# Performance work log

Measured on AMD Instinct MI355X. Metric: run time of the kernel, lower is better.

The kernel has to match this reference:

```python
import jax, jax.numpy as jnp
import numpy as np

N, P, D = 262144, 128, 64
EPS = 1e-5
NEG = -1e30


def setup_inputs() -> dict:
    key = jax.random.key(0)
    ks = jax.random.split(key, 12)
    feature = jax.random.normal(ks[0], (N, D), jnp.float32)
    feature_geo = jax.random.normal(ks[1], (N, D), jnp.float32)
    xyz = jax.random.uniform(ks[2], (N, 3), jnp.float32)
    centers = jax.random.uniform(ks[3], (3,), jnp.float32)
    plane_center = jax.random.uniform(ks[4], (P, 3), jnp.float32)
    nrm = jax.random.normal(ks[5], (P, 3), jnp.float32)
    plane_normal = nrm / jnp.linalg.norm(nrm, axis=1, keepdims=True)
    lo = 0.3 * jax.random.uniform(ks[6], (P, 3), jnp.float32)
    hi = 0.5 + 0.5 * jax.random.uniform(ks[7], (P, 3), jnp.float32)
    # exactly two active axes per plane (one axis of the aabb is zeroed)
    ax = jnp.arange(P) % 3
    keep = (jnp.arange(3)[None, :] != ax[:, None]).astype(jnp.float32)
    plane_xyz_min = lo * keep
    plane_xyz_max = hi * keep
    w1 = 0.05 * jax.random.normal(ks[8], (2 * D, D), jnp.float32)
    b1 = jnp.zeros((D,), jnp.float32)
    w2 = 0.05 * jax.random.normal(ks[9], (D, D), jnp.float32)
    b2 = jnp.zeros((D,), jnp.float32)
    w3 = 0.05 * jax.random.normal(ks[10], (D, 1), jnp.float32)
    b3 = jnp.zeros((1,), jnp.float32)
    g1 = jnp.ones((D,), jnp.float32); be1 = jnp.zeros((D,), jnp.float32)
    m1 = jnp.zeros((D,), jnp.float32); v1 = jnp.ones((D,), jnp.float32)
    g2 = jnp.ones((D,), jnp.float32); be2 = jnp.zeros((D,), jnp.float32)
    m2 = jnp.zeros((D,), jnp.float32); v2 = jnp.ones((D,), jnp.float32)
    return dict(feature=feature, feature_geo=feature_geo, xyz=xyz, centers=centers,
                plane_center=plane_center, plane_normal=plane_normal,
                plane_xyz_min=plane_xyz_min, plane_xyz_max=plane_xyz_max,
                w1=w1, b1=b1, g1=g1, be1=be1, m1=m1, v1=v1,
                w2=w2, b2=b2, g2=g2, be2=be2, m2=m2, v2=v2,
                w3=w3, b3=b3)


def _bn(x, g, b, m, v):
    return (x - m) * (g * jax.lax.rsqrt(v + EPS)) + b


def reference(feature, feature_geo, xyz, centers, plane_center, plane_normal,
              plane_xyz_min, plane_xyz_max, w1, b1, g1, be1, m1, v1,
              w2, b2, g2, be2, m2, v2, w3, b3):
    clouds = xyz + centers                                   # [N,3]
    f = jnp.concatenate([feature, feature_geo], axis=1)      # [N,2D]
    # 1x1 conv MLP == per-point matmul (fc1 -> fc2 with BN+ReLU, fc3)
    h1 = jax.nn.relu(_bn(f @ w1 + b1, g1, be1, m1, v1))      # [N,D]
    h2 = jax.nn.relu(_bn(h1 @ w2 + b2, g2, be2, m2, v2))     # [N,D]
    scores = jax.nn.relu(h2 @ w3 + b3)[:, 0]                 # [N]
    # per-plane aabb mask over the two active axes (xyz_max != 0)
    active = plane_xyz_max != 0                              # [P,3]
    in_rng = (clouds[None] >= plane_xyz_min[:, None]) & (clouds[None] < plane_xyz_max[:, None])
    range_mask = jnp.all(in_rng | ~active[:, None, :], axis=-1)   # [P,N]
    # point-to-plane distance: |(clouds - center) . normal|
    dots = clouds @ plane_normal.T                           # [N,P]
    offs = jnp.sum(plane_center * plane_normal, axis=1)      # [P]
    dist = jnp.abs(dots - offs[None, :]).T                   # [P,N]
    mask = range_mask & (dist < 0.1)                         # [P,N]
    sig = jax.nn.sigmoid(scores)                             # [N]
    on_mask = mask & (sig > 0.5)[None, :]
    off_mask = mask & (sig <= 0.5)[None, :]

    def pool(m):  # masked max-pool of fc2 features over points of one plane
        val = jnp.max(jnp.where(m[:, None], h2, NEG), axis=0)     # [D]
        return jnp.where(jnp.any(m), val, 0.0)

    on_feat = jax.lax.map(pool, on_mask)                     # [P,D]
    off_feat = jax.lax.map(pool, off_mask)                   # [P,D]
    scores_masked = jnp.where(mask, scores[None, :], 0.0)    # [P,N]
    return scores_masked, mask, on_mask, off_mask, on_feat, off_feat
```

## Files before the change

kernel.cpp:

```cpp
#include <hip/hip_runtime.h>
#include <hip/hip_bf16.h>
#include <math.h>

#define NPTS 262144
#define NP   128
#define DD   64
#define NWORDS (NPTS / 64)

#define AS4 __attribute__((address_space(4)))
typedef float evf4 __attribute__((ext_vector_type(4)));
typedef AS4 const float* csf;
typedef AS4 const evf4*  csf4;
#define TO_CSF(p)  ((csf)(unsigned long long)(const void*)(p))
#define TO_CSF4(p) ((csf4)(unsigned long long)(const void*)(p))

__global__ __launch_bounds__(256) void prep_kernel(
    const float* __restrict__ plane_center, const float* __restrict__ plane_normal,
    const float* __restrict__ pmin, const float* __restrict__ pmax,
    const float* __restrict__ w2,
    float* __restrict__ packed, float* __restrict__ w2T,
    float* __restrict__ out_feats)
{
    const int t = threadIdx.x;
    out_feats[blockIdx.x * 256 + t] = 0.0f;
    if (blockIdx.x == 0 && t < NP) {
        float n0 = plane_normal[t*3+0], n1 = plane_normal[t*3+1], n2 = plane_normal[t*3+2];
        float c0 = plane_center[t*3+0], c1 = plane_center[t*3+1], c2 = plane_center[t*3+2];
        float off = (c0*n0 + c1*n1) + c2*n2;
        float4* pp = reinterpret_cast<float4*>(packed) + t * 3;
        pp[0] = make_float4(n0, n1, n2, off);
        pp[1] = make_float4(pmin[t*3+0], pmin[t*3+1], pmin[t*3+2], 0.0f);
        pp[2] = make_float4(pmax[t*3+0], pmax[t*3+1], pmax[t*3+2], 0.0f);
    }
    if (blockIdx.x == 1) {
#pragma unroll
        for (int u = 0; u < 16; ++u) {
            const int e = u * 256 + t;
            const int j = e >> 6, k = e & 63;
            w2T[e] = w2[k * DD + j];
        }
    }
}

__global__ __launch_bounds__(256) void fused_kernel(
    const float* __restrict__ feature, const float* __restrict__ feature_geo,
    const float* __restrict__ xyz, const float* __restrict__ centers,
    const float* __restrict__ packed,
    const float* __restrict__ w1, const float* __restrict__ b1,
    const float* __restrict__ g1, const float* __restrict__ be1,
    const float* __restrict__ m1, const float* __restrict__ v1,
    const float* __restrict__ w2T, const float* __restrict__ b2,
    const float* __restrict__ g2, const float* __restrict__ be2,
    const float* __restrict__ m2, const float* __restrict__ v2,
    const float* __restrict__ w3, const float* __restrict__ b3,
    float* __restrict__ h2_out,
    float* __restrict__ out_sm, float* __restrict__ out_mask,
    float* __restrict__ out_on, float* __restrict__ out_off,
    unsigned long long* __restrict__ hitOn, unsigned long long* __restrict__ hitOff)
{
    __shared__ float sw1[128 * DD];
    __shared__ float sw2[DD * DD];
    const int t = threadIdx.x;
    const int bs = (blockIdx.x & 7) * 128 + (blockIdx.x >> 3);
    const int n = bs * 256 + t;
    const int lane = t & 63;
    const int word = n >> 6;

    {
        const float4* s1 = reinterpret_cast<const float4*>(w1);
        const float4* s2 = reinterpret_cast<const float4*>(w2T);
        float4* d1 = reinterpret_cast<float4*>(sw1);
        float4* d2 = reinterpret_cast<float4*>(sw2);
#pragma unroll
        for (int k = 0; k < 8; ++k) d1[t + k * 256] = s1[t + k * 256];
#pragma unroll
        for (int k = 0; k < 4; ++k) d2[t + k * 256] = s2[t + k * 256];
    }

    const csf cc = TO_CSF(centers);
    const float c0 = xyz[n*3+0] + cc[0];
    const float c1 = xyz[n*3+1] + cc[1];
    const float c2 = xyz[n*3+2] + cc[2];

    __syncthreads();

    float acc[DD];
#pragma unroll
    for (int j = 0; j < DD; ++j) acc[j] = 0.0f;

    const float4* fA = reinterpret_cast<const float4*>(feature) + (size_t)n * 16;
    const float4* fB = reinterpret_cast<const float4*>(feature_geo) + (size_t)n * 16;
#pragma unroll 1
    for (int q = 0; q < 16; ++q) {
        const float4 fv = fA[q];
        const evf4* wr = reinterpret_cast<const evf4*>(sw1 + q * 4 * DD);
#pragma unroll
        for (int j4 = 0; j4 < 16; ++j4) { const evf4 w = wr[j4];
            acc[4*j4+0] = fmaf(fv.x, w.x, acc[4*j4+0]);
            acc[4*j4+1] = fmaf(fv.x, w.y, acc[4*j4+1]);
            acc[4*j4+2] = fmaf(fv.x, w.z, acc[4*j4+2]);
            acc[4*j4+3] = fmaf(fv.x, w.w, acc[4*j4+3]); }
#pragma unroll
        for (int j4 = 0; j4 < 16; ++j4) { const evf4 w = wr[16 + j4];
            acc[4*j4+0] = fmaf(fv.y, w.x, acc[4*j4+0]);
            acc[4*j4+1] = fmaf(fv.y, w.y, acc[4*j4+1]);
            acc[4*j4+2] = fmaf(fv.y, w.z, acc[4*j4+2]);
            acc[4*j4+3] = fmaf(fv.y, w.w, acc[4*j4+3]); }
#pragma unroll
        for (int j4 = 0; j4 < 16; ++j4) { const evf4 w = wr[32 + j4];
            acc[4*j4+0] = fmaf(fv.z, w.x, acc[4*j4+0]);
            acc[4*j4+1] = fmaf(fv.z, w.y, acc[4*j4+1]);
            acc[4*j4+2] = fmaf(fv.z, w.z, acc[4*j4+2]);
            acc[4*j4+3] = fmaf(fv.z, w.w, acc[4*j4+3]); }
#pragma unroll
        for (int j4 = 0; j4 < 16; ++j4) { const evf4 w = wr[48 + j4];
            acc[4*j4+0] = fmaf(fv.w, w.x, acc[4*j4+0]);
            acc[4*j4+1] = fmaf(fv.w, w.y, acc[4*j4+1]);
            acc[4*j4+2] = fmaf(fv.w, w.z, acc[4*j4+2]);
            acc[4*j4+3] = fmaf(fv.w, w.w, acc[4*j4+3]); }
    }
#pragma unroll 1
    for (int q = 0; q < 16; ++q) {
        const float4 fv = fB[q];
        const evf4* wr = reinterpret_cast<const evf4*>(sw1 + (DD + q * 4) * DD);
#pragma unroll
        for (int j4 = 0; j4 < 16; ++j4) { const evf4 w = wr[j4];
            acc[4*j4+0] = fmaf(fv.x, w.x, acc[4*j4+0]);
            acc[4*j4+1] = fmaf(fv.x, w.y, acc[4*j4+1]);
            acc[4*j4+2] = fmaf(fv.x, w.z, acc[4*j4+2]);
            acc[4*j4+3] = fmaf(fv.x, w.w, acc[4*j4+3]); }
#pragma unroll
        for (int j4 = 0; j4 < 16; ++j4) { const evf4 w = wr[16 + j4];
            acc[4*j4+0] = fmaf(fv.y, w.x, acc[4*j4+0]);
            acc[4*j4+1] = fmaf(fv.y, w.y, acc[4*j4+1]);
            acc[4*j4+2] = fmaf(fv.y, w.z, acc[4*j4+2]);
            acc[4*j4+3] = fmaf(fv.y, w.w, acc[4*j4+3]); }
#pragma unroll
        for (int j4 = 0; j4 < 16; ++j4) { const evf4 w = wr[32 + j4];
            acc[4*j4+0] = fmaf(fv.z, w.x, acc[4*j4+0]);
            acc[4*j4+1] = fmaf(fv.z, w.y, acc[4*j4+1]);
            acc[4*j4+2] = fmaf(fv.z, w.z, acc[4*j4+2]);
            acc[4*j4+3] = fmaf(fv.z, w.w, acc[4*j4+3]); }
#pragma unroll
        for (int j4 = 0; j4 < 16; ++j4) { const evf4 w = wr[48 + j4];
            acc[4*j4+0] = fmaf(fv.w, w.x, acc[4*j4+0]);
            acc[4*j4+1] = fmaf(fv.w, w.y, acc[4*j4+1]);
            acc[4*j4+2] = fmaf(fv.w, w.z, acc[4*j4+2]);
            acc[4*j4+3] = fmaf(fv.w, w.w, acc[4*j4+3]); }
    }
    {
        const csf g1c = TO_CSF(g1), v1c = TO_CSF(v1), b1c = TO_CSF(b1),
                  m1c = TO_CSF(m1), be1c = TO_CSF(be1);
#pragma unroll
        for (int j = 0; j < DD; ++j) {
            float sc = g1c[j] * (1.0f / sqrtf(v1c[j] + 1e-5f));
            float h  = fmaf(acc[j] + b1c[j] - m1c[j], sc, be1c[j]);
            acc[j] = fmaxf(h, 0.0f);
        }
    }

    const csf g2c = TO_CSF(g2), v2c = TO_CSF(v2), b2c = TO_CSF(b2),
              m2c = TO_CSF(m2), be2c = TO_CSF(be2), w3c = TO_CSF(w3);
    float s = 0.0f;
    float4* o = reinterpret_cast<float4*>(h2_out) + (size_t)n * 16;
#pragma unroll 1
    for (int jq = 0; jq < 16; ++jq) {
        const evf4* r0 = reinterpret_cast<const evf4*>(sw2 + (4*jq + 0) * DD);
        const evf4* r1 = reinterpret_cast<const evf4*>(sw2 + (4*jq + 1) * DD);
        const evf4* r2 = reinterpret_cast<const evf4*>(sw2 + (4*jq + 2) * DD);
        const evf4* r3 = reinterpret_cast<const evf4*>(sw2 + (4*jq + 3) * DD);
        float a0 = 0.0f, a1 = 0.0f, a2 = 0.0f, a3 = 0.0f;
#pragma unroll
        for (int k4 = 0; k4 < 16; ++k4) {
            const evf4 w0 = r0[k4], w1v = r1[k4], w2v = r2[k4], w3v = r3[k4];
            const float h0 = acc[4*k4+0], h1v = acc[4*k4+1],
                        h2v = acc[4*k4+2], h3v = acc[4*k4+3];
            a0 = fmaf(h0, w0.x, a0); a0 = fmaf(h1v, w0.y, a0);
            a0 = fmaf(h2v, w0.z, a0); a0 = fmaf(h3v, w0.w, a0);
            a1 = fmaf(h0, w1v.x, a1); a1 = fmaf(h1v, w1v.y, a1);
            a1 = fmaf(h2v, w1v.z, a1); a1 = fmaf(h3v, w1v.w, a1);
            a2 = fmaf(h0, w2v.x, a2); a2 = fmaf(h1v, w2v.y, a2);
            a2 = fmaf(h2v, w2v.z, a2); a2 = fmaf(h3v, w2v.w, a2);
            a3 = fmaf(h0, w3v.x, a3); a3 = fmaf(h1v, w3v.y, a3);
            a3 = fmaf(h2v, w3v.z, a3); a3 = fmaf(h3v, w3v.w, a3);
        }
        float hv[4] = {a0, a1, a2, a3};
#pragma unroll
        for (int u = 0; u < 4; ++u) {
            const int jj = 4*jq + u;
            float sc = g2c[jj] * (1.0f / sqrtf(v2c[jj] + 1e-5f));
            float h  = fmaf(hv[u] + b2c[jj] - m2c[jj], sc, be2c[jj]);
            h = fmaxf(h, 0.0f);
            hv[u] = h;
            s = fmaf(h, w3c[jj], s);
        }
        o[jq] = make_float4(hv[0], hv[1], hv[2], hv[3]);
    }
    s += TO_CSF(b3)[0];
    const float score = fmaxf(s, 0.0f);

    const bool on = (0.5f + 0.5f * tanhf(0.5f * score)) > 0.5f;

    const csf4 pp = TO_CSF4(packed);
#pragma unroll 1
    for (int p = 0; p < NP; ++p) {
        const evf4 nrm = pp[p*3+0];
        const evf4 mn  = pp[p*3+1];
        const evf4 mx  = pp[p*3+2];
        float d = fabsf(fmaf(c2, nrm.z, fmaf(c1, nrm.y, c0 * nrm.x)) - nrm.w);
        bool ok0 = (mx.x == 0.0f) | ((c0 >= mn.x) & (c0 < mx.x));
        bool ok1 = (mx.y == 0.0f) | ((c1 >= mn.y) & (c1 < mx.y));
        bool ok2 = (mx.z == 0.0f) | ((c2 >= mn.z) & (c2 < mx.z));
        bool mk  = ok0 & ok1 & ok2 & (d < 0.1f);
        const size_t idx = (size_t)p * NPTS + n;
        const bool mon  = mk & on;
        const bool moff = mk & (!on);
        out_mask[idx] = mk ? 1.0f : 0.0f;
        out_sm[idx]   = mk ? score : 0.0f;
        out_on[idx]   = mon ? 1.0f : 0.0f;
        out_off[idx]  = moff ? 1.0f : 0.0f;
        unsigned long long bOn  = __ballot(mon);
        unsigned long long bOff = __ballot(moff);
        if (lane == 0) {
            hitOn [(size_t)p * NWORDS + word] = bOn;
            hitOff[(size_t)p * NWORDS + word] = bOff;
        }
    }
}

__global__ __launch_bounds__(256) void pool_kernel(
    const float* __restrict__ h2,
    const unsigned long long* __restrict__ hitOn,
    const unsigned long long* __restrict__ hitOff,
    int* __restrict__ out_feats_i)
{
    __shared__ float sacc[4][DD];
    const int t = threadIdx.x;
    const int lane = t & 63;
    const int wv = t >> 6;

    const int bid   = blockIdx.x;
    const int p     = bid >> 5;
    const int side  = (bid >> 4) & 1;
    const int chunk = bid & 15;
    const unsigned long long* hsrc = side ? hitOff : hitOn;

    const int wbase = chunk * 256 + wv * 64;
    const unsigned long long myw = hsrc[(size_t)p * NWORDS + wbase + lane];

    float acc = 0.0f;
    unsigned long long act = __ballot(myw != 0ULL);
    while (act) {
        const int l = __builtin_ctzll(act);
        act &= act - 1;
        unsigned long long w = __shfl(myw, l, 64);
        const size_t nbase = (size_t)(wbase + l) * 64;
        while (w) {
            const int b0 = __builtin_ctzll(w); w &= w - 1;
            if (w) {
                const int b1 = __builtin_ctzll(w); w &= w - 1;
                const float v0 = h2[(nbase + b0) * DD + lane];
                const float v1 = h2[(nbase + b1) * DD + lane];
                acc = fmaxf(acc, v0);
                acc = fmaxf(acc, v1);
            } else {
                const float v0 = h2[(nbase + b0) * DD + lane];
                acc = fmaxf(acc, v0);
            }
        }
    }

    sacc[wv][lane] = acc;
    __syncthreads();
    if (t < DD) {
        const float m = fmaxf(fmaxf(sacc[0][t], sacc[1][t]),
                              fmaxf(sacc[2][t], sacc[3][t]));
        if (m != 0.0f)
            atomicMax(&out_feats_i[side * NP * DD + p * DD + t], __float_as_int(m));
    }
}

extern "C" void kernel_launch(void* const* d_in, const int* in_sizes, int n_in,
                              void* d_out, int out_size, void* d_ws, size_t ws_size,
                              hipStream_t stream) {
    const float* feature      = (const float*)d_in[0];
    const float* feature_geo  = (const float*)d_in[1];
    const float* xyz          = (const float*)d_in[2];
    const float* centers      = (const float*)d_in[3];
    const float* plane_center = (const float*)d_in[4];
    const float* plane_normal = (const float*)d_in[5];
    const float* pmin         = (const float*)d_in[6];
    const float* pmax         = (const float*)d_in[7];
    const float* w1 = (const float*)d_in[8];
    const float* b1 = (const float*)d_in[9];
    const float* g1 = (const float*)d_in[10];
    const float* be1 = (const float*)d_in[11];
    const float* m1 = (const float*)d_in[12];
    const float* v1 = (const float*)d_in[13];
    const float* w2 = (const float*)d_in[14];
    const float* b2 = (const float*)d_in[15];
    const float* g2 = (const float*)d_in[16];
    const float* be2 = (const float*)d_in[17];
    const float* m2 = (const float*)d_in[18];
    const float* v2 = (const float*)d_in[19];
    const float* w3 = (const float*)d_in[20];
    const float* b3 = (const float*)d_in[21];

    float* out = (float*)d_out;
    const size_t PN = (size_t)NP * NPTS;
    float* out_sm    = out;
    float* out_mask  = out + PN;
    float* out_on    = out + 2 * PN;
    float* out_off   = out + 3 * PN;
    float* out_feats = out + 4 * PN;

    float* h2     = (float*)d_ws;
    unsigned long long* hitOn  = (unsigned long long*)(h2 + (size_t)NPTS * DD);
    unsigned long long* hitOff = hitOn + (size_t)NP * NWORDS;
    float* packed = (float*)(hitOff + (size_t)NP * NWORDS);
    float* w2T    = packed + NP * 12;

    prep_kernel<<<64, 256, 0, stream>>>(
        plane_center, plane_normal, pmin, pmax, w2, packed, w2T, out_feats);
    fused_kernel<<<NPTS / 256, 256, 0, stream>>>(
        feature, feature_geo, xyz, centers, packed,
        w1, b1, g1, be1, m1, v1, w2T, b2, g2, be2, m2, v2, w3, b3,
        h2, out_sm, out_mask, out_on, out_off, hitOn, hitOff);
    pool_kernel<<<4096, 256, 0, stream>>>(h2, hitOn, hitOff, (int*)out_feats);
}
```

Measured before the change: 804.2 us.

## Interleave plane-mask computation and mask stores into the fc1 GEMM loop

Computes the per-plane range/distance mask inside the fc1 accumulation loops, four planes per iteration, and writes out_mask there, so those stores overlap with the FMA-bound GEMM work. Mask bits are kept in two 64-bit registers and reused later for the score, on and off outputs. Plane parameters are staged in LDS instead of read through the constant path. This raises register pressure and LDS use, which could lower occupancy.

New measurement: 903.4 us. 1.12x slower.

```diff
diff --git a/kernel.cpp b/kernel.cpp
--- a/kernel.cpp
+++ b/kernel.cpp
@@ -41,6 +41,18 @@
         }
     }
 }
+
+#define C1PLANE(P, MKB) {                                                     \
+    const evf4 nrm = spk[(P)*3+0];                                            \
+    const evf4 mn  = spk[(P)*3+1];                                            \
+    const evf4 mx  = spk[(P)*3+2];                                            \
+    float d = fabsf(fmaf(c2, nrm.z, fmaf(c1, nrm.y, c0 * nrm.x)) - nrm.w);    \
+    bool ok0 = (mx.x == 0.0f) | ((c0 >= mn.x) & (c0 < mx.x));                 \
+    bool ok1 = (mx.y == 0.0f) | ((c1 >= mn.y) & (c1 < mx.y));                 \
+    bool ok2 = (mx.z == 0.0f) | ((c2 >= mn.z) & (c2 < mx.z));                 \
+    bool mk  = ok0 & ok1 & ok2 & (d < 0.1f);                                  \
+    out_mask[((size_t)(P) << 18) + n] = mk ? 1.0f : 0.0f;                     \
+    MKB |= ((unsigned long long)mk) << ((P) & 63); }
 
 __global__ __launch_bounds__(256) void fused_kernel(
     const float* __restrict__ feature, const float* __restrict__ feature_geo,
@@ -60,6 +72,7 @@
 {
     __shared__ float sw1[128 * DD];
     __shared__ float sw2[DD * DD];
+    __shared__ evf4  spk[NP * 3];
     const int t = threadIdx.x;
     const int bs = (blockIdx.x & 7) * 128 + (blockIdx.x >> 3);
     const int n = bs * 256 + t;
@@ -75,6 +88,10 @@
         for (int k = 0; k < 8; ++k) d1[t + k * 256] = s1[t + k * 256];
 #pragma unroll
         for (int k = 0; k < 4; ++k) d2[t + k * 256] = s2[t + k * 256];
+        const float4* sp = reinterpret_cast<const float4*>(packed);
+        float4* dp = reinterpret_cast<float4*>(spk);
+        dp[t] = sp[t];
+        if (t < 128) dp[256 + t] = sp[256 + t];
     }
 
     const csf cc = TO_CSF(centers);
@@ -87,6 +104,8 @@
     float acc[DD];
 #pragma unroll
     for (int j = 0; j < DD; ++j) acc[j] = 0.0f;
+
+    unsigned long long mkb0 = 0ULL, mkb1 = 0ULL;
 
     const float4* fA = reinterpret_cast<const float4*>(feature) + (size_t)n * 16;
     const float4* fB = reinterpret_cast<const float4*>(feature_geo) + (size_t)n * 16;
@@ -118,6 +137,10 @@
             acc[4*j4+1] = fmaf(fv.w, w.y, acc[4*j4+1]);
             acc[4*j4+2] = fmaf(fv.w, w.z, acc[4*j4+2]);
             acc[4*j4+3] = fmaf(fv.w, w.w, acc[4*j4+3]); }
+        C1PLANE(4*q + 0, mkb0)
+        C1PLANE(4*q + 1, mkb0)
+        C1PLANE(4*q + 2, mkb0)
+        C1PLANE(4*q + 3, mkb0)
     }
 #pragma unroll 1
     for (int q = 0; q < 16; ++q) {
@@ -147,6 +170,10 @@
             acc[4*j4+1] = fmaf(fv.w, w.y, acc[4*j4+1]);
             acc[4*j4+2] = fmaf(fv.w, w.z, acc[4*j4+2]);
             acc[4*j4+3] = fmaf(fv.w, w.w, acc[4*j4+3]); }
+        C1PLANE(64 + 4*q + 0, mkb1)
+        C1PLANE(64 + 4*q + 1, mkb1)
+        C1PLANE(64 + 4*q + 2, mkb1)
+        C1PLANE(64 + 4*q + 3, mkb1)
     }
     {
         const csf g1c = TO_CSF(g1), v1c = TO_CSF(v1), b1c = TO_CSF(b1),
@@ -201,21 +228,13 @@
 
     const bool on = (0.5f + 0.5f * tanhf(0.5f * score)) > 0.5f;
 
-    const csf4 pp = TO_CSF4(packed);
 #pragma unroll 1
     for (int p = 0; p < NP; ++p) {
-        const evf4 nrm = pp[p*3+0];
-        const evf4 mn  = pp[p*3+1];
-        const evf4 mx  = pp[p*3+2];
-        float d = fabsf(fmaf(c2, nrm.z, fmaf(c1, nrm.y, c0 * nrm.x)) - nrm.w);
-        bool ok0 = (mx.x == 0.0f) | ((c0 >= mn.x) & (c0 < mx.x));
-        bool ok1 = (mx.y == 0.0f) | ((c1 >= mn.y) & (c1 < mx.y));
-        bool ok2 = (mx.z == 0.0f) | ((c2 >= mn.z) & (c2 < mx.z));
-        bool mk  = ok0 & ok1 & ok2 & (d < 0.1f);
-        const size_t idx = (size_t)p * NPTS + n;
+        const unsigned long long wbits = (p & 64) ? mkb1 : mkb0;
+        const bool mk = (wbits >> (p & 63)) & 1ULL;
+        const size_t idx = ((size_t)p << 18) + n;
         const bool mon  = mk & on;
         const bool moff = mk & (!on);
-        out_mask[idx] = mk ? 1.0f : 0.0f;
         out_sm[idx]   = mk ? score : 0.0f;
         out_on[idx]   = mon ? 1.0f : 0.0f;
         out_off[idx]  = moff ? 1.0f : 0.0f;
```
